# Kernel tuning notes

Hardware: AMD Instinct MI355X
Metric: run time of the kernel (lower is better)

## Reference

```python
import jax, jax.numpy as jnp
import numpy as np

N_NODES, N_EDGES, WIDTH = 50000, 640000, 128


def setup_inputs() -> dict:
    key = jax.random.key(0)
    k1, k2, k3 = jax.random.split(key, 3)
    x = jax.random.normal(k1, (N_NODES, WIDTH), dtype=jnp.float32)
    e = jax.random.randint(k2, (2, N_EDGES), 0, N_NODES, dtype=jnp.int32)
    # LinearBlock(2*width, width): Linear(256 -> 128) + ReLU
    W = jax.random.normal(k3, (WIDTH, 2 * WIDTH), dtype=jnp.float32) * (1.0 / np.sqrt(2 * WIDTH))
    b = jnp.zeros((WIDTH,), dtype=jnp.float32)
    return {"x": x, "e": e, "W": W, "b": b}


def reference(x, e, W, b):
    src, dst = e[0], e[1]
    # gather-subtract: diffs[k] = x[dst_k] - x[src_k]  -> [E, width]
    diffs = x[dst] - x[src]
    n = x.shape[0]
    # scatter_max over destination nodes; torch_scatter leaves empty segments at 0
    maxes = jax.ops.segment_max(diffs, dst, num_segments=n)  # [N, width]
    deg = jax.ops.segment_sum(jnp.ones((dst.shape[0],), jnp.float32), dst, num_segments=n)
    maxes = jnp.where((deg > 0)[:, None], maxes, 0.0)
    # LinearBlock (Linear + ReLU) on concat, then residual
    h = jnp.concatenate([x, maxes], axis=1)  # [N, 2*width]
    return x + jax.nn.relu(h @ W.T + b)
```

## Files before the change

kernel.cpp:

```cpp
#include <hip/hip_runtime.h>
#include <hip/hip_bf16.h>

#define WIDTH   128
#define NNODES  50000
#define NEDGES  640000
#define NTILES  3125
#define NPAIRS  1563

#define RBLK    16
#define SSEG    8
#define RSZ     3125
#define SEG_I4  20000
#define C0      16
#define CAPB    128

#define BIN_BLOCKS  (RBLK * SSEG)
#define CVT_BLOCKS  1563
#define GRID_PREP   (BIN_BLOCKS + CVT_BLOCKS + 1)

#define MSTRIDE 136

typedef __attribute__((ext_vector_type(8))) short  short8;
typedef __attribute__((ext_vector_type(4))) short  short4_t;
typedef __attribute__((ext_vector_type(4))) float  float4_t;

__device__ inline short f2bf(float f) {
    union { float f; unsigned int u; } a;
    a.f = f;
    unsigned int r = a.u + 0x7FFFu + ((a.u >> 16) & 1u);
    return (short)(r >> 16);
}
__device__ inline unsigned int pack2bf(float a, float b) {
    unsigned int lo = (unsigned short)f2bf(a);
    unsigned int hi = (unsigned short)f2bf(b);
    return lo | (hi << 16);
}
__device__ inline float bflo(unsigned int u) { return __uint_as_float(u << 16); }
__device__ inline float bfhi(unsigned int u) { return __uint_as_float(u & 0xFFFF0000u); }

__global__ __launch_bounds__(1024) void prep_kernel(
    const float* __restrict__ x, const int* __restrict__ e,
    const float* __restrict__ W,
    uint2* __restrict__ xb2, uint2* __restrict__ wb2,
    int* __restrict__ counts2, int* __restrict__ buckets)
{
    __shared__ int cnt[RSZ];
    const int bid = blockIdx.x;
    const int tid = threadIdx.x;

    if (bid < BIN_BLOCKS) {
        int r = bid & (RBLK - 1);
        int s = bid >> 4;
        int base = r * RSZ;

        for (int i = tid; i < RSZ; i += 1024) cnt[i] = 0;
        __syncthreads();

        const int4* dst4 = (const int4*)(e + NEDGES + s * (SEG_I4 * 4));
        const int4* src4 = (const int4*)(e + s * (SEG_I4 * 4));

        int i = tid;
        int4 d = (i < SEG_I4) ? dst4[i] : make_int4(-1, -1, -1, -1);
        while (i < SEG_I4) {
            int inx = i + 1024;
            int4 dn = d;
            if (inx < SEG_I4) dn = dst4[inx];

            unsigned a0 = (unsigned)(d.x - base);
            unsigned a1 = (unsigned)(d.y - base);
            unsigned a2 = (unsigned)(d.z - base);
            unsigned a3 = (unsigned)(d.w - base);
            bool m0 = a0 < (unsigned)RSZ;
            bool m1 = a1 < (unsigned)RSZ;
            bool m2 = a2 < (unsigned)RSZ;
            bool m3 = a3 < (unsigned)RSZ;
            if (m0 | m1 | m2 | m3) {
                int4 sv = src4[i];
                if (m0) { int p = atomicAdd(&cnt[a0], 1); if (p < C0) buckets[d.x * CAPB + s * C0 + p] = sv.x; }
                if (m1) { int p = atomicAdd(&cnt[a1], 1); if (p < C0) buckets[d.y * CAPB + s * C0 + p] = sv.y; }
                if (m2) { int p = atomicAdd(&cnt[a2], 1); if (p < C0) buckets[d.z * CAPB + s * C0 + p] = sv.z; }
                if (m3) { int p = atomicAdd(&cnt[a3], 1); if (p < C0) buckets[d.w * CAPB + s * C0 + p] = sv.w; }
            }
            d = dn; i = inx;
        }
        __syncthreads();
        for (int i2 = tid; i2 < RSZ; i2 += 1024) {
            int c = cnt[i2]; if (c > C0) c = C0;
            counts2[(base + i2) * SSEG + s] = c;
        }
    } else if (bid < BIN_BLOCKS + CVT_BLOCKS) {
        int i = (bid - BIN_BLOCKS) * 1024 + tid;
        if (i < 1600000) {
            float4 v = ((const float4*)x)[i];
            uint2 p; p.x = pack2bf(v.x, v.y); p.y = pack2bf(v.z, v.w);
            xb2[i] = p;
        }
    } else {
        for (int j = tid; j < 8192; j += 1024) {
            float4 v = ((const float4*)W)[j];
            uint2 p; p.x = pack2bf(v.x, v.y); p.y = pack2bf(v.z, v.w);
            wb2[j] = p;
        }
    }
}

__global__ __launch_bounds__(256, 2) void gg_kernel(
    const float* __restrict__ x, const short* __restrict__ xb,
    const short* __restrict__ Wb, const float* __restrict__ b,
    const int* __restrict__ counts2, const int* __restrict__ buckets,
    float* __restrict__ out)
{
    __shared__ short maxLDS[32 * MSTRIDE];

    const int t     = threadIdx.x;
    const int wave  = t >> 6;
    const int lane  = t & 63;
    const int lm    = lane & 15;
    const int quad  = lane >> 4;
    const int nhalf = wave & 1;
    const int wpair = wave >> 1;
    const int ncol_base = nhalf * 64;
    const int h  = lane >> 5;
    const int cl = lane & 31;

    short8 bfrag[4][8];
#pragma unroll
    for (int nt = 0; nt < 4; ++nt) {
        int n = ncol_base + nt * 16 + lm;
#pragma unroll
        for (int kt = 0; kt < 8; ++kt) {
            int k = kt * 32 + quad * 8;
            bfrag[nt][kt] = *(const short8*)(Wb + n * 256 + k);
        }
    }
    float bias[4];
#pragma unroll
    for (int nt = 0; nt < 4; ++nt) bias[nt] = b[ncol_base + nt * 16 + lm];

#pragma unroll 1
    for (int p = blockIdx.x; p < NPAIRS; p += gridDim.x) {
        int nbase = p * 32;

#pragma unroll 1
        for (int i = 0; i < 8; ++i) {
            int ln   = wave * 8 + i;
            int node = nbase + ln;
            if (node < NNODES) {
                int s0 = lane >> 4;
                int j  = lane & 15;
                int c0 = counts2[node * SSEG + s0];
                int c1 = counts2[node * SSEG + 4 + s0];
                int idx0 = buckets[node * CAPB + lane];
                int idx1 = buckets[node * CAPB + 64 + lane];
                bool v0 = j < c0;
                bool v1 = j < c1;
                unsigned long long m0 = __ballot(v0);
                unsigned long long m1 = __ballot(v1);
                int p0 = __builtin_amdgcn_mbcnt_hi((unsigned)(m0 >> 32),
                         __builtin_amdgcn_mbcnt_lo((unsigned)m0, 0));
                int popc0 = __popcll(m0);
                int p1 = popc0 + __builtin_amdgcn_mbcnt_hi((unsigned)(m1 >> 32),
                                 __builtin_amdgcn_mbcnt_lo((unsigned)m1, 0));
                int deg = popc0 + __popcll(m1);
                int t0 = v0 ? p0 : 63;
                int t1 = v1 ? p1 : 63;
                int r0 = __builtin_amdgcn_ds_permute(t0 << 2, idx0);
                int r1 = __builtin_amdgcn_ds_permute(t1 << 2, idx1);
                int myidx = (lane < popc0) ? r0 : r1;

                float4 m; m.x = 3.4e38f; m.y = 3.4e38f; m.z = 3.4e38f; m.w = 3.4e38f;
#pragma unroll 1
                for (int j0 = 0; j0 < deg; j0 += 16) {
                    uint2 v[8];
#pragma unroll
                    for (int u = 0; u < 8; ++u) {
                        int jc = j0 + 2 * u + h;
                        jc = jc < deg ? jc : deg - 1;
                        int src = __shfl(myidx, jc);
                        v[u] = *(const uint2*)(xb + (size_t)src * WIDTH + cl * 4);
                    }
#pragma unroll
                    for (int u = 0; u < 8; ++u) {
                        m.x = fminf(m.x, bflo(v[u].x));
                        m.y = fminf(m.y, bfhi(v[u].x));
                        m.z = fminf(m.z, bflo(v[u].y));
                        m.w = fminf(m.w, bfhi(v[u].y));
                    }
                }
                m.x = fminf(m.x, __shfl_xor(m.x, 32));
                m.y = fminf(m.y, __shfl_xor(m.y, 32));
                m.z = fminf(m.z, __shfl_xor(m.z, 32));
                m.w = fminf(m.w, __shfl_xor(m.w, 32));

                if (h == 0) {
                    uint2 o;
                    if (deg > 0) {
                        uint2 xv = *(const uint2*)(xb + (size_t)node * WIDTH + cl * 4);
                        o.x = pack2bf(bflo(xv.x) - m.x, bfhi(xv.x) - m.y);
                        o.y = pack2bf(bflo(xv.y) - m.z, bfhi(xv.y) - m.w);
                    } else {
                        o.x = 0u; o.y = 0u;
                    }
                    *(uint2*)&maxLDS[ln * MSTRIDE + cl * 4] = o;
                }
            }
        }
        __syncthreads();

        int tile = p * 2 + wpair;
        if (tile < NTILES) {
            int row = tile * 16 + lm;
            const short* xbr = xb + (size_t)row * WIDTH;
            const short* mls = &maxLDS[(wpair * 16 + lm) * MSTRIDE];

            float4_t acc[4];
#pragma unroll
            for (int nt = 0; nt < 4; ++nt) { acc[nt].x = 0.f; acc[nt].y = 0.f; acc[nt].z = 0.f; acc[nt].w = 0.f; }

#pragma unroll
            for (int kt = 0; kt < 8; ++kt) {
                short8 afrag;
                if (kt < 4) {
                    afrag = *(const short8*)(xbr + kt * 32 + quad * 8);
                } else {
                    afrag = *(const short8*)(mls + (kt - 4) * 32 + quad * 8);
                }
#pragma unroll
                for (int nt = 0; nt < 4; ++nt) {
                    acc[nt] = __builtin_amdgcn_mfma_f32_16x16x32_bf16(
                        afrag, bfrag[nt][kt], acc[nt], 0, 0, 0);
                }
            }

#pragma unroll
            for (int nt = 0; nt < 4; ++nt) {
                int col = ncol_base + nt * 16 + lm;
#pragma unroll
                for (int r = 0; r < 4; ++r) {
                    int orow = tile * 16 + quad * 4 + r;
                    float v = acc[nt][r] + bias[nt];
                    v = v > 0.f ? v : 0.f;
                    size_t off = (size_t)orow * WIDTH + col;
                    out[off] = x[off] + v;
                }
            }
        }
        __syncthreads();
    }
}

__global__ __launch_bounds__(256) void fill_kernel(
    const int* __restrict__ e, int* __restrict__ counts, int* __restrict__ buckets)
{
    int i = blockIdx.x * 256 + threadIdx.x;
    if (i >= NEDGES) return;
    int src = e[i];
    int dst = e[NEDGES + i];
    int pos = atomicAdd(&counts[dst], 1);
    if (pos < 64) buckets[dst * 64 + pos] = src;
}

__global__ __launch_bounds__(256) void gather_min_fp32_kernel(
    const float* __restrict__ x, const int* __restrict__ counts,
    const int* __restrict__ buckets, unsigned int* __restrict__ maxes_u32)
{
    int wave = (blockIdx.x * 256 + threadIdx.x) >> 6;
    int lane = threadIdx.x & 63;
    if (wave >= NNODES) return;
    int node = wave;
    int deg  = counts[node];
    deg = deg > 64 ? 64 : deg;

    int myidx = (lane < deg) ? buckets[node * 64 + lane] : 0;
    int c = lane * 2;
    float2 m; m.x = 3.4e38f; m.y = 3.4e38f;
#pragma unroll 1
    for (int j0 = 0; j0 < deg; j0 += 8) {
        float2 v[8];
#pragma unroll
        for (int u = 0; u < 8; ++u) {
            int jc = j0 + u;
            jc = jc < deg ? jc : deg - 1;
            int src = __shfl(myidx, jc);
            v[u] = *(const float2*)(x + (size_t)src * WIDTH + c);
        }
#pragma unroll
        for (int u = 0; u < 8; ++u) {
            m.x = fminf(m.x, v[u].x);
            m.y = fminf(m.y, v[u].y);
        }
    }
    float2 o;
    if (deg > 0) {
        float2 xv = *(const float2*)(x + (size_t)node * WIDTH + c);
        o.x = xv.x - m.x;
        o.y = xv.y - m.y;
    } else { o.x = 0.f; o.y = 0.f; }
    maxes_u32[(size_t)node * 64 + lane] = pack2bf(o.x, o.y);
}

#define WLDS_STRIDE 264
__global__ __launch_bounds__(256, 2) void gemm_fallback_kernel(
    const float* __restrict__ x, const short* __restrict__ maxes,
    const float* __restrict__ W, const float* __restrict__ b,
    float* __restrict__ out)
{
    __shared__ short Wlds[WIDTH * WLDS_STRIDE];
    const int t = threadIdx.x;
#pragma unroll
    for (int i = 0; i < 32; ++i) {
        int idx4 = t + i * 256;
        int flat = idx4 << 2;
        float4 w = *(const float4*)(W + flat);
        int n = flat >> 8;
        int k = flat & 255;
        short4_t s;
        s.x = f2bf(w.x); s.y = f2bf(w.y); s.z = f2bf(w.z); s.w = f2bf(w.w);
        *(short4_t*)&Wlds[n * WLDS_STRIDE + k] = s;
    }
    __syncthreads();

    const int wave  = t >> 6;
    const int lane  = t & 63;
    const int lm    = lane & 15;
    const int quad  = lane >> 4;
    const int nhalf = wave & 1;
    const int wpair = wave >> 1;
    const int ncol_base = nhalf * 64;

    short8 bfrag[4][8];
#pragma unroll
    for (int nt = 0; nt < 4; ++nt) {
        int n = ncol_base + nt * 16 + lm;
#pragma unroll
        for (int kt = 0; kt < 8; ++kt) {
            int k = kt * 32 + quad * 8;
            bfrag[nt][kt] = *(const short8*)&Wlds[n * WLDS_STRIDE + k];
        }
    }

    const int stride = gridDim.x * 2;
#pragma unroll 1
    for (int tile = blockIdx.x * 2 + wpair; tile < NTILES; tile += stride) {
        int row = tile * 16 + lm;
        const float* xr = x     + (size_t)row * WIDTH;
        const short* mr = maxes + (size_t)row * WIDTH;

        float4_t acc[4];
#pragma unroll
        for (int nt = 0; nt < 4; ++nt) { acc[nt].x = 0.f; acc[nt].y = 0.f; acc[nt].z = 0.f; acc[nt].w = 0.f; }

#pragma unroll
        for (int kt = 0; kt < 8; ++kt) {
            int k = kt * 32 + quad * 8;
            short8 afrag;
            if (k < WIDTH) {
                float4 v0 = *(const float4*)(xr + k);
                float4 v1 = *(const float4*)(xr + k + 4);
                afrag[0] = f2bf(v0.x); afrag[1] = f2bf(v0.y);
                afrag[2] = f2bf(v0.z); afrag[3] = f2bf(v0.w);
                afrag[4] = f2bf(v1.x); afrag[5] = f2bf(v1.y);
                afrag[6] = f2bf(v1.z); afrag[7] = f2bf(v1.w);
            } else {
                afrag = *(const short8*)(mr + (k - WIDTH));
            }
#pragma unroll
            for (int nt = 0; nt < 4; ++nt) {
                acc[nt] = __builtin_amdgcn_mfma_f32_16x16x32_bf16(
                    afrag, bfrag[nt][kt], acc[nt], 0, 0, 0);
            }
        }

#pragma unroll
        for (int nt = 0; nt < 4; ++nt) {
            int col = ncol_base + nt * 16 + lm;
            float bias = b[col];
#pragma unroll
            for (int r = 0; r < 4; ++r) {
                int orow = tile * 16 + quad * 4 + r;
                float v = acc[nt][r] + bias;
                v = v > 0.f ? v : 0.f;
                size_t off = (size_t)orow * WIDTH + col;
                out[off] = x[off] + v;
            }
        }
    }
}

extern "C" void kernel_launch(void* const* d_in, const int* in_sizes, int n_in,
                              void* d_out, int out_size, void* d_ws, size_t ws_size,
                              hipStream_t stream) {
    const float* x = (const float*)d_in[0];
    const int*   e = (const int*)  d_in[1];
    const float* W = (const float*)d_in[2];
    const float* b = (const float*)d_in[3];
    float* out = (float*)d_out;

    char* ws = (char*)d_ws;

    const size_t off_buckets = 1600512;
    const size_t off_xb      = off_buckets + 25600000;
    const size_t off_wb      = off_xb + 12800000;
    const size_t need        = off_wb + 65536;

    if (ws_size >= need) {
        int*   counts2 = (int*)ws;
        int*   buckets = (int*)(ws + off_buckets);
        short* xb      = (short*)(ws + off_xb);
        short* wb      = (short*)(ws + off_wb);

        prep_kernel<<<GRID_PREP, 1024, 0, stream>>>(
            x, e, W, (uint2*)xb, (uint2*)wb, counts2, buckets);
        gg_kernel<<<512, 256, 0, stream>>>(
            x, xb, wb, b, counts2, buckets, out);
    } else {
        int*          counts  = (int*)ws;
        int*          buckets = (int*)(ws + 262144);
        unsigned int* maxes   = (unsigned int*)(ws + 262144 + 12800000);

        hipMemsetAsync(counts, 0, 262144, stream);
        fill_kernel<<<(NEDGES + 255) / 256, 256, 0, stream>>>(e, counts, buckets);
        gather_min_fp32_kernel<<<(NNODES + 3) / 4, 256, 0, stream>>>(
            x, counts, buckets, maxes);
        gemm_fallback_kernel<<<512, 256, 0, stream>>>(
            x, (const short*)maxes, W, b, out);
    }
}
```

Baseline: 170.1 us.

## Split fused gather-min/GEMM kernel into separate gather and GEMM kernels

Splits the fused kernel in two. The new gather kernel gives each node one wave across a large grid and writes the bf16 max features to a workspace buffer. A separate MFMA GEMM kernel then reads that buffer instead of LDS. This removes the per-block sync between the irregular gather phase and the GEMM phase and lets the gather run with much more parallelism, at the cost of an extra 12.8 MB global round-trip and one more kernel launch.

```diff
diff --git a/kernel.cpp b/kernel.cpp
--- a/kernel.cpp
+++ b/kernel.cpp
@@ -5,7 +5,6 @@
 #define NNODES  50000
 #define NEDGES  640000
 #define NTILES  3125
-#define NPAIRS  1563
 
 #define RBLK    16
 #define SSEG    8
@@ -17,8 +16,6 @@
 #define BIN_BLOCKS  (RBLK * SSEG)
 #define CVT_BLOCKS  1563
 #define GRID_PREP   (BIN_BLOCKS + CVT_BLOCKS + 1)
-
-#define MSTRIDE 136
 
 typedef __attribute__((ext_vector_type(8))) short  short8;
 typedef __attribute__((ext_vector_type(4))) short  short4_t;
@@ -104,14 +101,82 @@
     }
 }
 
-__global__ __launch_bounds__(256, 2) void gg_kernel(
+__global__ __launch_bounds__(256) void gather_min_bf16_kernel(
+    const uint2* __restrict__ xb2, const int* __restrict__ counts2,
+    const int* __restrict__ buckets, uint2* __restrict__ maxes2)
+{
+    int wave = (blockIdx.x * 256 + threadIdx.x) >> 6;
+    int lane = threadIdx.x & 63;
+    if (wave >= NNODES) return;
+    int node = wave;
+
+    int s0 = lane >> 4;
+    int j  = lane & 15;
+    int c0 = counts2[node * SSEG + s0];
+    int c1 = counts2[node * SSEG + 4 + s0];
+    int idx0 = buckets[node * CAPB + lane];
+    int idx1 = buckets[node * CAPB + 64 + lane];
+    bool v0 = j < c0;
+    bool v1 = j < c1;
+    unsigned long long m0 = __ballot(v0);
+    unsigned long long m1 = __ballot(v1);
+    int p0 = __builtin_amdgcn_mbcnt_hi((unsigned)(m0 >> 32),
+             __builtin_amdgcn_mbcnt_lo((unsigned)m0, 0));
+    int popc0 = __popcll(m0);
+    int p1 = popc0 + __builtin_amdgcn_mbcnt_hi((unsigned)(m1 >> 32),
+                     __builtin_amdgcn_mbcnt_lo((unsigned)m1, 0));
+    int deg = popc0 + __popcll(m1);
+    int t0 = v0 ? p0 : 63;
+    int t1 = v1 ? p1 : 63;
+    int r0 = __builtin_amdgcn_ds_permute(t0 << 2, idx0);
+    int r1 = __builtin_amdgcn_ds_permute(t1 << 2, idx1);
+    int myidx = (lane < popc0) ? r0 : r1;
+
+    int h  = lane >> 5;
+    int cl = lane & 31;
+
+    float4 m; m.x = 3.4e38f; m.y = 3.4e38f; m.z = 3.4e38f; m.w = 3.4e38f;
+#pragma unroll 1
+    for (int j0 = 0; j0 < deg; j0 += 16) {
+        uint2 v[8];
+#pragma unroll
+        for (int u = 0; u < 8; ++u) {
+            int jc = j0 + 2 * u + h;
+            jc = jc < deg ? jc : deg - 1;
+            int src = __shfl(myidx, jc);
+            v[u] = xb2[(size_t)src * 32 + cl];
+        }
+#pragma unroll
+        for (int u = 0; u < 8; ++u) {
+            m.x = fminf(m.x, bflo(v[u].x));
+            m.y = fminf(m.y, bfhi(v[u].x));
+            m.z = fminf(m.z, bflo(v[u].y));
+            m.w = fminf(m.w, bfhi(v[u].y));
+        }
+    }
+    m.x = fminf(m.x, __shfl_xor(m.x, 32));
+    m.y = fminf(m.y, __shfl_xor(m.y, 32));
+    m.z = fminf(m.z, __shfl_xor(m.z, 32));
+    m.w = fminf(m.w, __shfl_xor(m.w, 32));
+
+    if (h == 0) {
+        uint2 o;
+        if (deg > 0) {
+            uint2 xv = xb2[(size_t)node * 32 + cl];
+            o.x = pack2bf(bflo(xv.x) - m.x, bfhi(xv.x) - m.y);
+            o.y = pack2bf(bflo(xv.y) - m.z, bfhi(xv.y) - m.w);
+        } else {
+            o.x = 0u; o.y = 0u;
+        }
+        maxes2[(size_t)node * 32 + cl] = o;
+    }
+}
+
+__global__ __launch_bounds__(256, 2) void gemm_kernel(
     const float* __restrict__ x, const short* __restrict__ xb,
-    const short* __restrict__ Wb, const float* __restrict__ b,
-    const int* __restrict__ counts2, const int* __restrict__ buckets,
-    float* __restrict__ out)
-{
-    __shared__ short maxLDS[32 * MSTRIDE];
-
+    const short* __restrict__ maxes, const short* __restrict__ Wb,
+    const float* __restrict__ b, float* __restrict__ out)
+{
     const int t     = threadIdx.x;
     const int wave  = t >> 6;
     const int lane  = t & 63;
@@ -120,8 +185,6 @@
     const int nhalf = wave & 1;
     const int wpair = wave >> 1;
     const int ncol_base = nhalf * 64;
-    const int h  = lane >> 5;
-    const int cl = lane & 31;
 
     short8 bfrag[4][8];
 #pragma unroll
@@ -137,115 +200,41 @@
 #pragma unroll
     for (int nt = 0; nt < 4; ++nt) bias[nt] = b[ncol_base + nt * 16 + lm];
 
+    const int stride = gridDim.x * 2;
 #pragma unroll 1
-    for (int p = blockIdx.x; p < NPAIRS; p += gridDim.x) {
-        int nbase = p * 32;
-
-#pragma unroll 1
-        for (int i = 0; i < 8; ++i) {
-            int ln   = wave * 8 + i;
-            int node = nbase + ln;
-            if (node < NNODES) {
-                int s0 = lane >> 4;
-                int j  = lane & 15;
-                int c0 = counts2[node * SSEG + s0];
-                int c1 = counts2[node * SSEG + 4 + s0];
-                int idx0 = buckets[node * CAPB + lane];
-                int idx1 = buckets[node * CAPB + 64 + lane];
-                bool v0 = j < c0;
-                bool v1 = j < c1;
-                unsigned long long m0 = __ballot(v0);
-                unsigned long long m1 = __ballot(v1);
-                int p0 = __builtin_amdgcn_mbcnt_hi((unsigned)(m0 >> 32),
-                         __builtin_amdgcn_mbcnt_lo((unsigned)m0, 0));
-                int popc0 = __popcll(m0);
-                int p1 = popc0 + __builtin_amdgcn_mbcnt_hi((unsigned)(m1 >> 32),
-                                 __builtin_amdgcn_mbcnt_lo((unsigned)m1, 0));
-                int deg = popc0 + __popcll(m1);
-                int t0 = v0 ? p0 : 63;
-                int t1 = v1 ? p1 : 63;
-                int r0 = __builtin_amdgcn_ds_permute(t0 << 2, idx0);
-                int r1 = __builtin_amdgcn_ds_permute(t1 << 2, idx1);
-                int myidx = (lane < popc0) ? r0 : r1;
-
-                float4 m; m.x = 3.4e38f; m.y = 3.4e38f; m.z = 3.4e38f; m.w = 3.4e38f;
-#pragma unroll 1
-                for (int j0 = 0; j0 < deg; j0 += 16) {
-                    uint2 v[8];
-#pragma unroll
-                    for (int u = 0; u < 8; ++u) {
-                        int jc = j0 + 2 * u + h;
-                        jc = jc < deg ? jc : deg - 1;
-                        int src = __shfl(myidx, jc);
-                        v[u] = *(const uint2*)(xb + (size_t)src * WIDTH + cl * 4);
-                    }
-#pragma unroll
-                    for (int u = 0; u < 8; ++u) {
-                        m.x = fminf(m.x, bflo(v[u].x));
-                        m.y = fminf(m.y, bfhi(v[u].x));
-                        m.z = fminf(m.z, bflo(v[u].y));
-                        m.w = fminf(m.w, bfhi(v[u].y));
-                    }
-                }
-                m.x = fminf(m.x, __shfl_xor(m.x, 32));
-                m.y = fminf(m.y, __shfl_xor(m.y, 32));
-                m.z = fminf(m.z, __shfl_xor(m.z, 32));
-                m.w = fminf(m.w, __shfl_xor(m.w, 32));
-
-                if (h == 0) {
-                    uint2 o;
-                    if (deg > 0) {
-                        uint2 xv = *(const uint2*)(xb + (size_t)node * WIDTH + cl * 4);
-                        o.x = pack2bf(bflo(xv.x) - m.x, bfhi(xv.x) - m.y);
-                        o.y = pack2bf(bflo(xv.y) - m.z, bfhi(xv.y) - m.w);
-                    } else {
-                        o.x = 0u; o.y = 0u;
-                    }
-                    *(uint2*)&maxLDS[ln * MSTRIDE + cl * 4] = o;
-                }
-            }
-        }
-        __syncthreads();
-
-        int tile = p * 2 + wpair;
-        if (tile < NTILES) {
-            int row = tile * 16 + lm;
-            const short* xbr = xb + (size_t)row * WIDTH;
-            const short* mls = &maxLDS[(wpair * 16 + lm) * MSTRIDE];
-
-            float4_t acc[4];
-#pragma unroll
-            for (int nt = 0; nt < 4; ++nt) { acc[nt].x = 0.f; acc[nt].y = 0.f; acc[nt].z = 0.f; acc[nt].w = 0.f; }
-
-#pragma unroll
-            for (int kt = 0; kt < 8; ++kt) {
-                short8 afrag;
-                if (kt < 4) {
-                    afrag = *(const short8*)(xbr + kt * 32 + quad * 8);
-                } else {
-                    afrag = *(const short8*)(mls + (kt - 4) * 32 + quad * 8);
-                }
-#pragma unroll
-                for (int nt = 0; nt < 4; ++nt) {
-                    acc[nt] = __builtin_amdgcn_mfma_f32_16x16x32_bf16(
-                        afrag, bfrag[nt][kt], acc[nt], 0, 0, 0);
-                }
-            }
-
+    for (int tile = blockIdx.x * 2 + wpair; tile < NTILES; tile += stride) {
+        int row = tile * 16 + lm;
+        const short* xbr = xb    + (size_t)row * WIDTH;
+        const short* mr  = maxes + (size_t)row * WIDTH;
+
+        float4_t acc[4];
+#pragma unroll
+        for (int nt = 0; nt < 4; ++nt) { acc[nt].x = 0.f; acc[nt].y = 0.f; acc[nt].z = 0.f; acc[nt].w = 0.f; }
+
+#pragma unroll
+        for (int kt = 0; kt < 8; ++kt) {
+            short8 afrag;
+            if (kt < 4) afrag = *(const short8*)(xbr + kt * 32 + quad * 8);
+            else        afrag = *(const short8*)(mr + (kt - 4) * 32 + quad * 8);
 #pragma unroll
             for (int nt = 0; nt < 4; ++nt) {
-                int col = ncol_base + nt * 16 + lm;
-#pragma unroll
-                for (int r = 0; r < 4; ++r) {
-                    int orow = tile * 16 + quad * 4 + r;
-                    float v = acc[nt][r] + bias[nt];
-                    v = v > 0.f ? v : 0.f;
-                    size_t off = (size_t)orow * WIDTH + col;
-                    out[off] = x[off] + v;
-                }
-            }
-        }
-        __syncthreads();
+                acc[nt] = __builtin_amdgcn_mfma_f32_16x16x32_bf16(
+                    afrag, bfrag[nt][kt], acc[nt], 0, 0, 0);
+            }
+        }
+
+#pragma unroll
+        for (int nt = 0; nt < 4; ++nt) {
+            int col = ncol_base + nt * 16 + lm;
+#pragma unroll
+            for (int r = 0; r < 4; ++r) {
+                int orow = tile * 16 + quad * 4 + r;
+                float v = acc[nt][r] + bias[nt];
+                v = v > 0.f ? v : 0.f;
+                size_t off = (size_t)orow * WIDTH + col;
+                out[off] = x[off] + v;
+            }
+        }
     }
 }
 
@@ -399,20 +388,24 @@
     char* ws = (char*)d_ws;
 
     const size_t off_buckets = 1600512;
-    const size_t off_xb      = off_buckets + 25600000;
+    const size_t off_maxes   = off_buckets + 25600000;
+    const size_t off_xb      = off_maxes + 12800000;
     const size_t off_wb      = off_xb + 12800000;
     const size_t need        = off_wb + 65536;
 
     if (ws_size >= need) {
-        int*   counts2 = (int*)ws;
-        int*   buckets = (int*)(ws + off_buckets);
-        short* xb      = (short*)(ws + off_xb);
-        short* wb      = (short*)(ws + off_wb);
+        int*          counts2 = (int*)ws;
+        int*          buckets = (int*)(ws + off_buckets);
+        unsigned int* maxes   = (unsigned int*)(ws + off_maxes);
+        short*        xb      = (short*)(ws + off_xb);
+        short*        wb      = (short*)(ws + off_wb);
 
         prep_kernel<<<GRID_PREP, 1024, 0, stream>>>(
             x, e, W, (uint2*)xb, (uint2*)wb, counts2, buckets);
-        gg_kernel<<<512, 256, 0, stream>>>(
-            x, xb, wb, b, counts2, buckets, out);
+        gather_min_bf16_kernel<<<(NNODES + 3) / 4, 256, 0, stream>>>(
+            (const uint2*)xb, counts2, buckets, (uint2*)maxes);
+        gemm_kernel<<<512, 256, 0, stream>>>(
+            x, xb, (const short*)maxes, wb, b, out);
     } else {
         int*          counts  = (int*)ws;
         int*          buckets = (int*)(ws + 262144);
```

Result: faster. 149.1 us (-12.4%).
